# Optimization experiments

Hardware: AMD Instinct MI355X
Metric: run time of the kernel (lower is better)

The kernel has to match this reference:

```python
import jax, jax.numpy as jnp
import numpy as np

B, T, C, H = 256, 512, 64, 512


def _init(key, shape, scale=0.05):
    return jax.random.normal(key, shape, dtype=jnp.float32) * scale


def setup_inputs() -> dict:
    key = jax.random.key(0)
    ks = jax.random.split(key, 12)
    return {
        "x": jax.random.normal(ks[0], (B, T, C), dtype=jnp.float32),
        # encoder GRU params (PyTorch layout: W_ih [3H, C], W_hh [3H, H])
        "enc_Wih": _init(ks[1], (3 * H, C)),
        "enc_Whh": _init(ks[2], (3 * H, H)),
        "enc_bih": _init(ks[3], (3 * H,)),
        "enc_bhh": _init(ks[4], (3 * H,)),
        # decoder GRU params
        "dec_Wih": _init(ks[5], (3 * H, C)),
        "dec_Whh": _init(ks[6], (3 * H, H)),
        "dec_bih": _init(ks[7], (3 * H,)),
        "dec_bhh": _init(ks[8], (3 * H,)),
        # output projection
        "Wout": _init(ks[9], (C, H)),
        "bout": _init(ks[10], (C,)),
    }


def _gru_cell(gi, h, Whh, bhh):
    # PyTorch GRU math: r,z,n gate order
    gh = h @ Whh.T + bhh
    ir, iz, inn = jnp.split(gi, 3, axis=-1)
    hr, hz, hn = jnp.split(gh, 3, axis=-1)
    r = jax.nn.sigmoid(ir + hr)
    z = jax.nn.sigmoid(iz + hz)
    n = jnp.tanh(inn + r * hn)
    return (1.0 - z) * n + z * h


def reference(x, enc_Wih, enc_Whh, enc_bih, enc_bhh,
              dec_Wih, dec_Whh, dec_bih, dec_bhh, Wout, bout):
    b, t, c = x.shape
    hdim = enc_Whh.shape[1]
    # ---- encoder: single full-sequence GRU, return final hidden ----
    xs = jnp.swapaxes(x, 0, 1)                      # [T, B, C]
    gi_all = xs @ enc_Wih.T + enc_bih               # precompute input gates [T, B, 3H]

    def enc_step(h, gi):
        return _gru_cell(gi, h, enc_Whh, enc_bhh), None

    h0 = jnp.zeros((b, hdim), dtype=x.dtype)
    h_enc, _ = jax.lax.scan(enc_step, h0, gi_all)

    # ---- decoder: free-running (eval mode, teacher_forcing_ratio=0) ----
    start = jnp.zeros((b, c), dtype=x.dtype)        # zero start token

    def dec_step(carry, _):
        prev, h = carry
        gi = prev @ dec_Wih.T + dec_bih
        h_new = _gru_cell(gi, h, dec_Whh, dec_bhh)
        pred = h_new @ Wout.T + bout                # [B, C]
        return (pred, h_new), pred

    _, preds = jax.lax.scan(dec_step, (start, h_enc), None, length=t)
    return jnp.swapaxes(preds, 0, 1)                # [B, T, C]
```

## Files before the change

### kernel.cpp

```cpp
#include <hip/hip_runtime.h>
#include <hip/hip_bf16.h>


#define B_ 256
#define T_ 512
#define C_ 64
#define H_ 512
#define TC_ 32768
#define BH_ 131072

typedef __attribute__((ext_vector_type(8))) short s16x8;
typedef __attribute__((ext_vector_type(4))) float f32x4;
typedef __attribute__((ext_vector_type(4))) unsigned int u32x4;

__device__ __forceinline__ unsigned short f2b(float f) {
    unsigned int u = __float_as_uint(f);
    unsigned int r = (u + 0x7FFFu + ((u >> 16) & 1u)) >> 16;
    return (unsigned short)r;
}
__device__ __forceinline__ float sigm(float v) {
    return __builtin_amdgcn_rcpf(1.f + __expf(-v));
}
__device__ __forceinline__ float ftanh(float v) {
    float a = fabsf(v);
    float e = __expf(-2.f * a);
    float t = (1.f - e) * __builtin_amdgcn_rcpf(1.f + e);
    return copysignf(t, v);
}
template<bool FAST>
__device__ __forceinline__ s16x8 ldh16x(const unsigned short* p) {
    u32x4 r;
    if constexpr (FAST)
        asm volatile("global_load_dwordx4 %0, %1, off sc0" : "=v"(r) : "v"(p));
    else
        asm volatile("global_load_dwordx4 %0, %1, off sc0 sc1" : "=v"(r) : "v"(p));
    return __builtin_bit_cast(s16x8, r);
}
template<bool FAST>
__device__ __forceinline__ void sth16x(unsigned short* p, u32x4 v) {
    if constexpr (FAST)
        asm volatile("global_store_dwordx4 %0, %1, off sc0" :: "v"(p), "v"(v) : "memory");
    else
        asm volatile("global_store_dwordx4 %0, %1, off sc0 sc1" :: "v"(p), "v"(v) : "memory");
}


__global__ __launch_bounds__(256) void prep_enc_k(
    const float* __restrict__ Wih, const float* __restrict__ Whh,
    const float* __restrict__ bih, const float* __restrict__ bhh,
    unsigned short* __restrict__ W, float* __restrict__ bias)
{
    int idx = blockIdx.x * 256 + threadIdx.x;
    if (idx >= 2048 * 576) return;
    int n = idx / 576, k = idx % 576;
    int part = (n >> 4) & 3, jc = n & 15, j16 = n >> 6;
    int j = j16 * 16 + jc;
    float v;
    if (part == 0)      v = (k < 64) ? Wih[j * 64 + k]          : Whh[(size_t)j * 512 + (k - 64)];
    else if (part == 1) v = (k < 64) ? Wih[(512 + j) * 64 + k]  : Whh[(size_t)(512 + j) * 512 + (k - 64)];
    else if (part == 2) v = (k < 64) ? Wih[(1024 + j) * 64 + k] : 0.f;
    else                v = (k < 64) ? 0.f                       : Whh[(size_t)(1024 + j) * 512 + (k - 64)];
    W[(size_t)n * 576 + k] = f2b(v);
    if (k == 0) {
        float b;
        if (part == 0)      b = bih[j] + bhh[j];
        else if (part == 1) b = bih[512 + j] + bhh[512 + j];
        else if (part == 2) b = bih[1024 + j];
        else                b = bhh[1024 + j];
        bias[n] = b;
    }
}

__global__ __launch_bounds__(256) void prep_dec_k(
    const float* __restrict__ Wih, const float* __restrict__ Whh,
    const float* __restrict__ Wout,
    unsigned short* __restrict__ W1, unsigned short* __restrict__ W0)
{
    int n = blockIdx.x;
    __shared__ float wrow[64];
    bool isout = (n >= 2048);
    int part = 0, j = 0, n3 = 0;
    if (!isout) {
        part = (n >> 4) & 3;
        int jc = n & 15, j16 = n >> 6;
        j = j16 * 16 + jc;
        n3 = (part == 0) ? j : (part == 1) ? (512 + j) : (1024 + j);
    }
    if (threadIdx.x < 64 && !isout && part != 3)
        wrow[threadIdx.x] = Wih[n3 * 64 + threadIdx.x];
    __syncthreads();
    for (int kk = 0; kk < 2; ++kk) {
        int k = kk * 256 + threadIdx.x;
        float v1, v0;
        if (isout) {
            v1 = v0 = Wout[(size_t)(n - 2048) * 512 + k];
        } else if (part == 3) {
            v1 = v0 = Whh[(size_t)(1024 + j) * 512 + k];
        } else {
            float af = 0.f;
            #pragma unroll
            for (int c = 0; c < 64; ++c) af += wrow[c] * Wout[(size_t)c * 512 + k];
            if (part == 2) { v1 = af; v0 = 0.f; }
            else { float wh = Whh[(size_t)n3 * 512 + k]; v1 = af + wh; v0 = wh; }
        }
        W1[(size_t)n * 512 + k] = f2b(v1);
        W0[(size_t)n * 512 + k] = f2b(v0);
    }
}

__global__ __launch_bounds__(256) void prep_dec_bias_k(
    const float* __restrict__ Wih, const float* __restrict__ bih,
    const float* __restrict__ bhh, const float* __restrict__ bout,
    float* __restrict__ b1, float* __restrict__ b0)
{
    int n = blockIdx.x * 256 + threadIdx.x;
    if (n >= 2112) return;
    if (n >= 2048) { b1[n] = bout[n - 2048]; b0[n] = bout[n - 2048]; return; }
    int part = (n >> 4) & 3, jc = n & 15, j16 = n >> 6;
    int j = j16 * 16 + jc;
    float v1, v0;
    if (part == 3) { v1 = v0 = bhh[1024 + j]; }
    else {
        int n3 = (part == 0) ? j : (part == 1) ? (512 + j) : (1024 + j);
        float wib = 0.f;
        #pragma unroll
        for (int c = 0; c < 64; ++c) wib += Wih[n3 * 64 + c] * bout[c];
        if (part == 2) { v1 = bih[1024 + j] + wib; v0 = bih[1024 + j]; }
        else { float base = bih[n3] + bhh[n3]; v1 = base + wib; v0 = base; }
    }
    b1[n] = v1; b0[n] = v0;
}


template<bool SLEEP>
__device__ __forceinline__ void wait_flags64(const unsigned int* fl, int lane, unsigned int tgt) {
    const unsigned int* fp = fl + lane * 32;
    while (true) {
        unsigned int fv = __hip_atomic_load(fp, __ATOMIC_RELAXED, __HIP_MEMORY_SCOPE_AGENT);
        if (__all(fv >= tgt)) break;
        if (SLEEP) __builtin_amdgcn_s_sleep(1);
    }
    asm volatile("" ::: "memory");
    __builtin_amdgcn_sched_barrier(0);
}

template<int NK, bool PRED, bool FAST>
__device__ __forceinline__ void do_step(
    const unsigned short* __restrict__ hin, unsigned short* __restrict__ hout,
    const s16x8 (&bfr)[36], const s16x8 (&pfr)[8], const float4 (&xf)[2][2],
    const float* bR, float bp, float (&h32)[4],
    float* __restrict__ out, int tout,
    unsigned int* __restrict__ flagp, int step,
    int r0, int j, int kh, int rh, int lane, bool duty,
    float (*Ored)[64][28], unsigned short (*Hst)[16][24])
{
    constexpr int HK = NK / 2;
    const int jc = lane & 15, kq = lane >> 4;
    const int ks0 = kh * HK;
    const unsigned short* hrow = hin + (size_t)(r0 + rh * 16 + jc) * H_;

    s16x8 af[HK];
    if (NK == 18 && kh == 0) {
        #pragma unroll
        for (int i2 = 0; i2 < 2; ++i2) {
            s16x8 v;
            v[0] = (short)f2b(xf[i2][0].x); v[1] = (short)f2b(xf[i2][0].y);
            v[2] = (short)f2b(xf[i2][0].z); v[3] = (short)f2b(xf[i2][0].w);
            v[4] = (short)f2b(xf[i2][1].x); v[5] = (short)f2b(xf[i2][1].y);
            v[6] = (short)f2b(xf[i2][1].z); v[7] = (short)f2b(xf[i2][1].w);
            af[i2] = v;
        }
    }
    #pragma unroll
    for (int i = 0; i < HK; ++i) {
        const int gks = ks0 + i;
        const bool isx = (NK == 18) && (gks < 2);
        if (!isx) {
            const int hk = ((NK == 18) ? (gks - 2) : gks) * 32 + kq * 8;
            af[i] = ldh16x<FAST>(hrow + hk);
        }
    }
    asm volatile("s_waitcnt vmcnt(0)" ::: "memory");
    __builtin_amdgcn_sched_barrier(0);

    f32x4 acc[4] = {{0,0,0,0},{0,0,0,0},{0,0,0,0},{0,0,0,0}};
    f32x4 pacc = {0,0,0,0};
    #pragma unroll
    for (int i = 0; i < HK; ++i) {
        #pragma unroll
        for (int q = 0; q < 4; ++q)
            acc[q] = __builtin_amdgcn_mfma_f32_16x16x32_bf16(af[i], bfr[i * 4 + q], acc[q], 0, 0, 0);
        if (PRED && duty)
            pacc = __builtin_amdgcn_mfma_f32_16x16x32_bf16(af[i], pfr[i], pacc, 0, 0, 0);
    }

    if (kh == 1) {
        #pragma unroll
        for (int q = 0; q < 4; ++q) *(f32x4*)&Ored[rh][lane][q * 4] = acc[q];
        if (PRED && duty) *(f32x4*)&Ored[rh][lane][16] = pacc;
    }
    asm volatile("s_waitcnt lgkmcnt(0)" ::: "memory");
    __builtin_amdgcn_s_barrier();
    __builtin_amdgcn_sched_barrier(0);

    if (kh == 0) {
        #pragma unroll
        for (int q = 0; q < 4; ++q) {
            f32x4 o = *(const f32x4*)&Ored[rh][lane][q * 4];
            acc[q] = acc[q] + o;
        }
        if (PRED && duty) {
            f32x4 o = *(const f32x4*)&Ored[rh][lane][16];
            pacc = pacc + o;
        }
        float hn[4];
        #pragma unroll
        for (int r = 0; r < 4; ++r) {
            float gr = acc[0][r] + bR[0];
            float gz = acc[1][r] + bR[1];
            float gi = acc[2][r] + bR[2];
            float gh = acc[3][r] + bR[3];
            float rg = sigm(gr), zg = sigm(gz);
            float ng = ftanh(gi + rg * gh);
            hn[r] = (1.f - zg) * ng + zg * h32[r];
            h32[r] = hn[r];
        }
        #pragma unroll
        for (int r = 0; r < 4; ++r) Hst[rh][kq * 4 + r][jc] = f2b(hn[r]);
        asm volatile("s_waitcnt lgkmcnt(0)" ::: "memory");
        __builtin_amdgcn_sched_barrier(0);
        if (lane < 32) {
            const int row = lane >> 1, hh = lane & 1;
            u32x4 hv = *(const u32x4*)&Hst[rh][row][hh * 8];
            sth16x<FAST>(hout + (size_t)(r0 + rh * 16 + row) * H_ + j * 16 + hh * 8, hv);
        }
        asm volatile("s_waitcnt vmcnt(0)" ::: "memory");
        if (lane == 0)
            __hip_atomic_store(flagp, (unsigned int)(step + 1),
                               __ATOMIC_RELAXED, __HIP_MEMORY_SCOPE_AGENT);
        if (PRED && duty) {
            #pragma unroll
            for (int r = 0; r < 4; ++r)
                out[(size_t)(r0 + rh * 16 + kq * 4 + r) * TC_ + (size_t)tout * C_ + j * 16 + jc] = pacc[r] + bp;
        }
    }
}

template<bool FAST>
__device__ __forceinline__ void persist_body(
    const unsigned short* __restrict__ WdecT,
    const unsigned short* __restrict__ Wdec0T,
    const float* __restrict__ x,
    unsigned short* __restrict__ h16,
    float* __restrict__ out,
    unsigned int* __restrict__ fl,
    s16x8 (&bfr)[36], s16x8 (&pfr)[8],
    const float (&be)[4], const float (&bd)[4], const float (&bd0)[4], float bp,
    int r0, int j, int w, int kh, int rh, int lane, bool duty,
    float (*Ored)[64][28], unsigned short (*Hst)[16][24])
{
    const int jc = lane & 15, kq = lane >> 4;
    unsigned int* flagp = fl + (j * 2 + rh) * 32;
    float h32[4] = {0.f, 0.f, 0.f, 0.f};
    int parity = 0;
    float4 xf[2][2];

    for (int step = 0; step < 1024; ++step) {
        const bool enc = step < 512;
        if (enc && kh == 0) {
            const float* xp = x + (size_t)(r0 + rh * 16 + jc) * TC_ + (size_t)step * C_ + kq * 8;
            #pragma unroll
            for (int i2 = 0; i2 < 2; ++i2) {
                xf[i2][0] = *(const float4*)(xp + i2 * 32);
                xf[i2][1] = *(const float4*)(xp + i2 * 32 + 4);
            }
        }
        if (step == 512) {
            #pragma unroll
            for (int i = 0; i < 8; ++i) {
                const int gks = kh * 8 + i;
                #pragma unroll
                for (int q = 0; q < 4; ++q)
                    bfr[i * 4 + q] = *(const s16x8*)(Wdec0T + (size_t)(j * 64 + q * 16 + jc) * 512 + gks * 32 + kq * 8);
                if (duty)
                    pfr[i] = *(const s16x8*)(WdecT + (size_t)(2048 + j * 16 + jc) * 512 + gks * 32 + kq * 8);
            }
        } else if (step == 513) {
            #pragma unroll
            for (int i = 0; i < 8; ++i) {
                const int gks = kh * 8 + i;
                #pragma unroll
                for (int q = 0; q < 4; ++q)
                    bfr[i * 4 + q] = *(const s16x8*)(WdecT + (size_t)(j * 64 + q * 16 + jc) * 512 + gks * 32 + kq * 8);
            }
        }
        if (step > 0) {
            if (w == 1) wait_flags64<false>(fl, lane, (unsigned int)step);
            __builtin_amdgcn_s_barrier();
            __builtin_amdgcn_sched_barrier(0);
        }

        const unsigned short* hin = h16 + (size_t)parity * BH_;
        unsigned short* hout = h16 + (size_t)(parity ^ 1) * BH_;

        if (enc)
            do_step<18, false, FAST>(hin, hout, bfr, pfr, xf, be,  bp, h32, out, 0,
                                     flagp, step, r0, j, kh, rh, lane, duty, Ored, Hst);
        else if (step == 512)
            do_step<16, false, FAST>(hin, hout, bfr, pfr, xf, bd0, bp, h32, out, 0,
                                     flagp, step, r0, j, kh, rh, lane, duty, Ored, Hst);
        else
            do_step<16, true,  FAST>(hin, hout, bfr, pfr, xf, bd,  bp, h32, out, step - 513,
                                     flagp, step, r0, j, kh, rh, lane, duty, Ored, Hst);

        parity ^= 1;
    }

    if (duty) {
        wait_flags64<true>(fl, lane, 1024u);
        const unsigned short* hin = h16 + (size_t)parity * BH_;
        const unsigned short* hrow = hin + (size_t)(r0 + rh * 16 + jc) * H_;
        s16x8 hf[8];
        #pragma unroll
        for (int i = 0; i < 8; ++i) {
            const int gks = kh * 8 + i;
            hf[i] = ldh16x<FAST>(hrow + gks * 32 + kq * 8);
        }
        asm volatile("s_waitcnt vmcnt(0)" ::: "memory");
        __builtin_amdgcn_sched_barrier(0);
        f32x4 pacc = {0, 0, 0, 0};
        #pragma unroll
        for (int i = 0; i < 8; ++i)
            pacc = __builtin_amdgcn_mfma_f32_16x16x32_bf16(hf[i], pfr[i], pacc, 0, 0, 0);
        if (kh == 1) *(f32x4*)&Ored[rh][lane][16] = pacc;
        asm volatile("s_waitcnt lgkmcnt(0)" ::: "memory");
        __builtin_amdgcn_s_barrier();
        __builtin_amdgcn_sched_barrier(0);
        if (kh == 0) {
            f32x4 o = *(const f32x4*)&Ored[rh][lane][16];
            pacc = pacc + o;
            #pragma unroll
            for (int r = 0; r < 4; ++r)
                out[(size_t)(r0 + rh * 16 + kq * 4 + r) * TC_ + (size_t)511 * C_ + j * 16 + jc] = pacc[r] + bp;
        }
    }
}

__global__ __launch_bounds__(256, 1) void gru_persist(
    const unsigned short* __restrict__ WencT,
    const unsigned short* __restrict__ WdecT,
    const unsigned short* __restrict__ Wdec0T,
    const float* __restrict__ benc, const float* __restrict__ bdec, const float* __restrict__ bdec0,
    const float* __restrict__ x,
    unsigned short* __restrict__ h16,
    float* __restrict__ out,
    unsigned int* __restrict__ flags,
    unsigned int* __restrict__ xcdslot)
{
    __shared__ __align__(16) float Ored[2][64][28];
    __shared__ __align__(16) unsigned short Hst[2][16][24];

    const int bid = blockIdx.x;
    const int g = bid & 7, j = bid >> 3;
    const int tid = threadIdx.x;
    const int w = tid >> 6, lane = tid & 63;
    const int kh = w & 1, rh = w >> 1;
    const int jc = lane & 15, kq = lane >> 4;
    const int r0 = g * 32;
    const bool duty = (j < 4);
    unsigned int* fl = flags + g * 64 * 32;

    unsigned int xcc;
    asm volatile("s_getreg_b32 %0, hwreg(HW_REG_XCC_ID)" : "=s"(xcc));
    if (tid == 0)
        __hip_atomic_store(xcdslot + bid, xcc + 1u, __ATOMIC_RELAXED, __HIP_MEMORY_SCOPE_AGENT);

    float be[4], bd[4], bd0[4];
    #pragma unroll
    for (int q = 0; q < 4; ++q) {
        be[q]  = benc[j * 64 + q * 16 + jc];
        bd[q]  = bdec[j * 64 + q * 16 + jc];
        bd0[q] = bdec0[j * 64 + q * 16 + jc];
    }
    const float bp = duty ? bdec[2048 + j * 16 + jc] : 0.f;

    s16x8 bfr[36];
    #pragma unroll
    for (int i = 0; i < 9; ++i) {
        const int gks = kh * 9 + i;
        #pragma unroll
        for (int q = 0; q < 4; ++q)
            bfr[i * 4 + q] = *(const s16x8*)(WencT + (size_t)(j * 64 + q * 16 + jc) * 576 + gks * 32 + kq * 8);
    }
    s16x8 pfr[8];
    #pragma unroll
    for (int i = 0; i < 8; ++i) pfr[i] = s16x8{0,0,0,0,0,0,0,0};

    unsigned int mv;
    {
        const unsigned int* sp = xcdslot + (((lane & 31) << 3) + g);
        while (true) {
            mv = __hip_atomic_load(sp, __ATOMIC_RELAXED, __HIP_MEMORY_SCOPE_AGENT);
            if (!__any(mv == 0u)) break;
            __builtin_amdgcn_s_sleep(2);
        }
    }
    const bool fast = __all(mv == __builtin_amdgcn_readfirstlane(mv));

    if (fast)
        persist_body<true>(WdecT, Wdec0T, x, h16, out, fl, bfr, pfr,
                           be, bd, bd0, bp, r0, j, w, kh, rh, lane, duty, Ored, Hst);
    else
        persist_body<false>(WdecT, Wdec0T, x, h16, out, fl, bfr, pfr,
                            be, bd, bd0, bp, r0, j, w, kh, rh, lane, duty, Ored, Hst);
}


extern "C" void kernel_launch(void* const* d_in, const int* in_sizes, int n_in,
                              void* d_out, int out_size, void* d_ws, size_t ws_size,
                              hipStream_t stream) {
    const float* x    = (const float*)d_in[0];
    const float* eWih = (const float*)d_in[1];
    const float* eWhh = (const float*)d_in[2];
    const float* ebih = (const float*)d_in[3];
    const float* ebhh = (const float*)d_in[4];
    const float* dWih = (const float*)d_in[5];
    const float* dWhh = (const float*)d_in[6];
    const float* dbih = (const float*)d_in[7];
    const float* dbhh = (const float*)d_in[8];
    const float* Wout = (const float*)d_in[9];
    const float* bout = (const float*)d_in[10];

    size_t off = 0;
    auto carve = [&](size_t bytes) -> void* {
        off = (off + 255) & ~(size_t)255;
        void* p = (char*)d_ws + off;
        off += bytes;
        return p;
    };
    unsigned short* WencT  = (unsigned short*)carve((size_t)2048 * 576 * 2);
    unsigned short* WdecT  = (unsigned short*)carve((size_t)2112 * 512 * 2);
    unsigned short* Wdec0T = (unsigned short*)carve((size_t)2112 * 512 * 2);
    float* benc  = (float*)carve(2048 * 4);
    float* bdec  = (float*)carve(2112 * 4);
    float* bdec0 = (float*)carve(2112 * 4);
    unsigned short* h16 = (unsigned short*)carve((size_t)2 * BH_ * 2);
    unsigned int* flags = (unsigned int*)carve(8 * 64 * 32 * 4);
    unsigned int* xcdslot = (unsigned int*)carve(256 * 4);

    hipMemsetAsync(h16, 0, (size_t)2 * BH_ * 2, stream);
    hipMemsetAsync(flags, 0, 8 * 64 * 32 * 4, stream);
    hipMemsetAsync(xcdslot, 0, 256 * 4, stream);

    prep_enc_k<<<(2048 * 576 + 255) / 256, 256, 0, stream>>>(eWih, eWhh, ebih, ebhh, WencT, benc);
    prep_dec_k<<<2112, 256, 0, stream>>>(dWih, dWhh, Wout, WdecT, Wdec0T);
    prep_dec_bias_k<<<9, 256, 0, stream>>>(dWih, dbih, dbhh, bout, bdec, bdec0);

    gru_persist<<<256, 256, 0, stream>>>(WencT, WdecT, Wdec0T, benc, bdec, bdec0,
                                         x, h16, (float*)d_out, flags, xcdslot);
}
```

Before: 3.578 ms.

## Consolidate per-block hidden-state store and flag signal; poll flags with cheaper loads

Each block now publishes its hidden-state slice with a single wave after a workgroup barrier, and sets one flag per block instead of one per row-half. This halves the number of flags every consumer polls. On the fast (same-XCD) path, flag stores and most poll loads use sc0-only global accesses, with a periodic agent-scope atomic load as a fallback. The goal is lower inter-block synchronization latency on each recurrent step, at the cost of an extra s_barrier per step and a weaker coherence assumption on the fast path.

```diff
diff --git a/kernel.cpp b/kernel.cpp
--- a/kernel.cpp
+++ b/kernel.cpp
@@ -27,6 +27,7 @@
     float t = (1.f - e) * __builtin_amdgcn_rcpf(1.f + e);
     return copysignf(t, v);
 }
+
 template<bool FAST>
 __device__ __forceinline__ s16x8 ldh16x(const unsigned short* p) {
     u32x4 r;
@@ -42,6 +43,19 @@
         asm volatile("global_store_dwordx4 %0, %1, off sc0" :: "v"(p), "v"(v) : "memory");
     else
         asm volatile("global_store_dwordx4 %0, %1, off sc0 sc1" :: "v"(p), "v"(v) : "memory");
+}
+template<bool FAST>
+__device__ __forceinline__ void stflag(unsigned int* p, unsigned int v) {
+    if constexpr (FAST)
+        asm volatile("global_store_dword %0, %1, off sc0" :: "v"(p), "v"(v) : "memory");
+    else
+        __hip_atomic_store(p, v, __ATOMIC_RELAXED, __HIP_MEMORY_SCOPE_AGENT);
+}
+__device__ __forceinline__ unsigned int ldflag_sc0(const unsigned int* p) {
+    unsigned int r;
+    asm volatile("global_load_dword %0, %1, off sc0" : "=v"(r) : "v"(p));
+    asm volatile("s_waitcnt vmcnt(0)" ::: "memory");
+    return r;
 }
 
 
@@ -132,11 +146,16 @@
 }
 
 
-template<bool SLEEP>
-__device__ __forceinline__ void wait_flags64(const unsigned int* fl, int lane, unsigned int tgt) {
-    const unsigned int* fp = fl + lane * 32;
+template<bool FAST, bool SLEEP>
+__device__ __forceinline__ void wait_flags32(const unsigned int* fl, int lane, unsigned int tgt) {
+    const unsigned int* fp = fl + (lane & 31) * 32;
+    unsigned int it = 0;
     while (true) {
-        unsigned int fv = __hip_atomic_load(fp, __ATOMIC_RELAXED, __HIP_MEMORY_SCOPE_AGENT);
+        unsigned int fv;
+        if (FAST && ((++it) & 15u) != 0u)
+            fv = ldflag_sc0(fp);
+        else
+            fv = __hip_atomic_load(fp, __ATOMIC_RELAXED, __HIP_MEMORY_SCOPE_AGENT);
         if (__all(fv >= tgt)) break;
         if (SLEEP) __builtin_amdgcn_s_sleep(1);
     }
@@ -227,22 +246,23 @@
         }
         #pragma unroll
         for (int r = 0; r < 4; ++r) Hst[rh][kq * 4 + r][jc] = f2b(hn[r]);
-        asm volatile("s_waitcnt lgkmcnt(0)" ::: "memory");
-        __builtin_amdgcn_sched_barrier(0);
-        if (lane < 32) {
-            const int row = lane >> 1, hh = lane & 1;
-            u32x4 hv = *(const u32x4*)&Hst[rh][row][hh * 8];
-            sth16x<FAST>(hout + (size_t)(r0 + rh * 16 + row) * H_ + j * 16 + hh * 8, hv);
-        }
+    }
+    asm volatile("s_waitcnt lgkmcnt(0)" ::: "memory");
+    __builtin_amdgcn_s_barrier();
+    __builtin_amdgcn_sched_barrier(0);
+
+    if (kh == 0 && rh == 0) {
+        const int row = lane >> 1, half = lane & 1;
+        u32x4 hv = *(const u32x4*)&Hst[row >> 4][row & 15][half * 8];
+        sth16x<FAST>(hout + (size_t)(r0 + row) * H_ + j * 16 + half * 8, hv);
         asm volatile("s_waitcnt vmcnt(0)" ::: "memory");
         if (lane == 0)
-            __hip_atomic_store(flagp, (unsigned int)(step + 1),
-                               __ATOMIC_RELAXED, __HIP_MEMORY_SCOPE_AGENT);
-        if (PRED && duty) {
-            #pragma unroll
-            for (int r = 0; r < 4; ++r)
-                out[(size_t)(r0 + rh * 16 + kq * 4 + r) * TC_ + (size_t)tout * C_ + j * 16 + jc] = pacc[r] + bp;
-        }
+            stflag<FAST>(flagp, (unsigned int)(step + 1));
+    }
+    if (PRED && kh == 0 && duty) {
+        #pragma unroll
+        for (int r = 0; r < 4; ++r)
+            out[(size_t)(r0 + rh * 16 + kq * 4 + r) * TC_ + (size_t)tout * C_ + j * 16 + jc] = pacc[r] + bp;
     }
 }
 
@@ -253,14 +273,13 @@
     const float* __restrict__ x,
     unsigned short* __restrict__ h16,
     float* __restrict__ out,
-    unsigned int* __restrict__ fl,
+    unsigned int* __restrict__ fl, unsigned int* __restrict__ flagp,
     s16x8 (&bfr)[36], s16x8 (&pfr)[8],
     const float (&be)[4], const float (&bd)[4], const float (&bd0)[4], float bp,
     int r0, int j, int w, int kh, int rh, int lane, bool duty,
     float (*Ored)[64][28], unsigned short (*Hst)[16][24])
 {
     const int jc = lane & 15, kq = lane >> 4;
-    unsigned int* flagp = fl + (j * 2 + rh) * 32;
     float h32[4] = {0.f, 0.f, 0.f, 0.f};
     int parity = 0;
     float4 xf[2][2];
@@ -295,7 +314,7 @@
             }
         }
         if (step > 0) {
-            if (w == 1) wait_flags64<false>(fl, lane, (unsigned int)step);
+            if (w == 1) wait_flags32<FAST, false>(fl, lane, (unsigned int)step);
             __builtin_amdgcn_s_barrier();
             __builtin_amdgcn_sched_barrier(0);
         }
@@ -317,7 +336,7 @@
     }
 
     if (duty) {
-        wait_flags64<true>(fl, lane, 1024u);
+        wait_flags32<FAST, true>(fl, lane, 1024u);
         const unsigned short* hin = h16 + (size_t)parity * BH_;
         const unsigned short* hrow = hin + (size_t)(r0 + rh * 16 + jc) * H_;
         s16x8 hf[8];
@@ -368,7 +387,8 @@
     const int jc = lane & 15, kq = lane >> 4;
     const int r0 = g * 32;
     const bool duty = (j < 4);
-    unsigned int* fl = flags + g * 64 * 32;
+    unsigned int* fl = flags + g * 32 * 32;
+    unsigned int* flagp = fl + j * 32;
 
     unsigned int xcc;
     asm volatile("s_getreg_b32 %0, hwreg(HW_REG_XCC_ID)" : "=s"(xcc));
@@ -408,10 +428,10 @@
     const bool fast = __all(mv == __builtin_amdgcn_readfirstlane(mv));
 
     if (fast)
-        persist_body<true>(WdecT, Wdec0T, x, h16, out, fl, bfr, pfr,
+        persist_body<true>(WdecT, Wdec0T, x, h16, out, fl, flagp, bfr, pfr,
                            be, bd, bd0, bp, r0, j, w, kh, rh, lane, duty, Ored, Hst);
     else
-        persist_body<false>(WdecT, Wdec0T, x, h16, out, fl, bfr, pfr,
+        persist_body<false>(WdecT, Wdec0T, x, h16, out, fl, flagp, bfr, pfr,
                             be, bd, bd0, bp, r0, j, w, kh, rh, lane, duty, Ored, Hst);
 }
 
@@ -445,11 +465,11 @@
     float* bdec  = (float*)carve(2112 * 4);
     float* bdec0 = (float*)carve(2112 * 4);
     unsigned short* h16 = (unsigned short*)carve((size_t)2 * BH_ * 2);
-    unsigned int* flags = (unsigned int*)carve(8 * 64 * 32 * 4);
+    unsigned int* flags = (unsigned int*)carve(8 * 32 * 32 * 4);
     unsigned int* xcdslot = (unsigned int*)carve(256 * 4);
 
     hipMemsetAsync(h16, 0, (size_t)2 * BH_ * 2, stream);
-    hipMemsetAsync(flags, 0, 8 * 64 * 32 * 4, stream);
+    hipMemsetAsync(flags, 0, 8 * 32 * 32 * 4, stream);
     hipMemsetAsync(xcdslot, 0, 256 * 4, stream);
 
     prep_enc_k<<<(2048 * 576 + 255) / 256, 256, 0, stream>>>(eWih, eWhh, ebih, ebhh, WencT, benc);
```

New measurement: 3.847 ms. 1.08x slower.
